# Kernel optimization log

Hardware: AMD Instinct MI355X
Metric: run time of the kernel (lower is better)

## Reference

```python
import jax, jax.numpy as jnp
import numpy as np

B, S, I, H = 64, 512, 512, 1024


def setup_inputs() -> dict:
    key = jax.random.key(0)
    ks = jax.random.split(key, 14)
    bound = (1.0 / H) ** 0.5
    u = lambda k, shape: jax.random.uniform(k, shape, jnp.float32, -bound, bound)
    return {
        "inputs": jax.random.normal(ks[0], (B, S, I), jnp.float32),
        "hidden_states": jax.random.normal(ks[1], (1, B, H), jnp.float32),
        "w_ir": u(ks[2], (H, I)), "w_iz": u(ks[3], (H, I)), "w_in": u(ks[4], (H, I)),
        "b_ir": u(ks[5], (H,)), "b_iz": u(ks[6], (H,)), "b_in": u(ks[7], (H,)),
        "w_hr": u(ks[8], (H, H)), "w_hz": u(ks[9], (H, H)), "w_hn": u(ks[10], (H, H)),
        "b_hr": u(ks[11], (H,)), "b_hz": u(ks[12], (H,)), "b_hn": u(ks[13], (H,)),
    }


def gru_forward(inputs, hidden_states, w_ir, w_iz, w_in, b_ir, b_iz, b_in,
                w_hr, w_hz, w_hn, b_hr, b_hz, b_hn):
    h0 = hidden_states[0]  # (B, H)
    # Original loop starts at t=1, so inputs[:, 0] is unused.
    x = inputs[:, 1:]  # (B, S-1, I)
    # Precompute all input projections (cuDNN-style), then scan the recurrence.
    xr = jnp.einsum('bsi,hi->sbh', x, w_ir) + b_ir
    xz = jnp.einsum('bsi,hi->sbh', x, w_iz) + b_iz
    xn = jnp.einsum('bsi,hi->sbh', x, w_in) + b_in

    def step(h, xs):
        xr_t, xz_t, xn_t = xs
        r = jax.nn.sigmoid(xr_t + h @ w_hr.T + b_hr)
        n = jnp.tanh(xn_t + r * (h @ w_hn.T + b_hn))
        z = jax.nn.sigmoid(xz_t + h @ w_hz.T + b_hz)
        h = (1.0 - z) * n + z * h
        return h, h

    h_last, hs = jax.lax.scan(step, h0, (xr, xz, xn))  # hs: (S-1, B, H)
    outputs = jnp.concatenate([h0[None], hs], axis=0).swapaxes(0, 1)  # (B, S, H)
    return outputs, h_last[None]  # final hidden keeps leading dim 1


def reference(inputs, hidden_states, w_ir, w_iz, w_in, b_ir, b_iz, b_in,
              w_hr, w_hz, w_hn, b_hr, b_hz, b_hn):
    return gru_forward(inputs, hidden_states, w_ir, w_iz, w_in, b_ir, b_iz, b_in,
                       w_hr, w_hz, w_hn, b_hr, b_hz, b_hn)
```

## Files before the change

### kernel.cpp

```cpp
#include <hip/hip_runtime.h>
#include <hip/hip_bf16.h>

typedef __bf16 bf16x8 __attribute__((ext_vector_type(8)));
typedef float  f32x4  __attribute__((ext_vector_type(4)));
typedef unsigned long long ull;

#define Bq 64
#define Sq 512
#define Iq 512
#define Hq 1024
#define TSTEPS 511
#define MB 16
#define NCOLS 32
#define SHq (Sq*Hq)
#define TAGM 0x0001000100010001ull

__device__ inline unsigned short f2bf(float f){ return __builtin_bit_cast(unsigned short, (__bf16)f); }

__device__ inline unsigned ah_addr(unsigned row, unsigned k){ return ((row<<11) + (k<<1)) ^ ((row&7)<<4); }
__device__ inline unsigned ax_addr(unsigned row, unsigned k){ return ((row<<10) + (k<<1)) ^ ((row&7)<<4); }

__device__ inline bf16x8 load_wfrag(const float* p){
  float4 a = *(const float4*)p;
  float4 b = *(const float4*)(p+4);
  bf16x8 w;
  w[0]=(__bf16)a.x; w[1]=(__bf16)a.y; w[2]=(__bf16)a.z; w[3]=(__bf16)a.w;
  w[4]=(__bf16)b.x; w[5]=(__bf16)b.y; w[6]=(__bf16)b.z; w[7]=(__bf16)b.w;
  return w;
}

#define KEEP(v_) asm volatile("" : "+v"(v_))

__global__ __launch_bounds__(512, 1) void gru_kernel(
    const float* __restrict__ x, const float* __restrict__ h0,
    const float* __restrict__ w_ir, const float* __restrict__ w_iz, const float* __restrict__ w_in_,
    const float* __restrict__ b_ir, const float* __restrict__ b_iz, const float* __restrict__ b_in_,
    const float* __restrict__ w_hr, const float* __restrict__ w_hz, const float* __restrict__ w_hn,
    const float* __restrict__ b_hr, const float* __restrict__ b_hz, const float* __restrict__ b_hn,
    float* __restrict__ out, void* ws)
{
  __shared__ unsigned short Ah[MB*Hq];
  __shared__ unsigned short Ax[MB*Iq];
  __shared__ float P[8*2048];
  __shared__ float biasR[NCOLS], biasZ[NCOLS], biasNX[NCOLS], biasNH[NCOLS];

  const unsigned tid    = threadIdx.x;
  const unsigned bid    = blockIdx.x;
  const unsigned g      = bid & 3;
  const unsigned colbase= (bid >> 2) * NCOLS;
  const unsigned lane   = tid & 63;
  const unsigned w      = tid >> 6;
  const unsigned l15    = lane & 15;
  const unsigned l4     = lane >> 4;

  unsigned short* hb0 = (unsigned short*)ws;
  unsigned short* hb1 = hb0 + Bq*Hq;

  if (tid < NCOLS) {
    unsigned c = colbase + tid;
    biasR[tid]  = b_ir[c] + b_hr[c];
    biasZ[tid]  = b_iz[c] + b_hz[c];
    biasNX[tid] = b_in_[c];
    biasNH[tid] = b_hn[c];
  }

  const unsigned ctr = tid >> 8, Lr = (tid >> 2) & 63, ir = tid & 3;
  const unsigned rrow = ((Lr >> 4) << 2) + ir;
  const unsigned rcol = ctr*16 + (Lr & 15);
  float hold;
  {
    unsigned b = g*MB + rrow, hcol = colbase + rcol;
    hold = h0[(size_t)b*Hq + hcol];
    out[(size_t)b*SHq + hcol] = hold;
    unsigned short u = (unsigned short)(f2bf(hold) & ~1u);
    __hip_atomic_store(hb0 + (size_t)b*Hq + hcol, u,
                       __ATOMIC_RELAXED, __HIP_MEMORY_SCOPE_AGENT);
  }

  bf16x8 wRX[2][2], wZX[2][2], wNX[2][2];
  bf16x8 wRH[2][4], wZH[2][4], wNH[2][4];
  #pragma unroll
  for (int ct = 0; ct < 2; ++ct) {
    const unsigned hcf = colbase + ct*16 + l15;
    #pragma unroll
    for (int j = 0; j < 2; ++j) {
      unsigned off = (w*2 + j)*32 + l4*8;
      wRX[ct][j] = load_wfrag(w_ir  + (size_t)hcf*Iq + off);
      wZX[ct][j] = load_wfrag(w_iz  + (size_t)hcf*Iq + off);
      wNX[ct][j] = load_wfrag(w_in_ + (size_t)hcf*Iq + off);
      KEEP(wRX[ct][j]); KEEP(wZX[ct][j]); KEEP(wNX[ct][j]);
    }
    #pragma unroll
    for (int j = 0; j < 4; ++j) {
      unsigned off = (w*4 + j)*32 + l4*8;
      wRH[ct][j] = load_wfrag(w_hr + (size_t)hcf*Hq + off);
      wZH[ct][j] = load_wfrag(w_hz + (size_t)hcf*Hq + off);
      wNH[ct][j] = load_wfrag(w_hn + (size_t)hcf*Hq + off);
      KEEP(wRH[ct][j]); KEEP(wZH[ct][j]); KEEP(wNH[ct][j]);
    }
  }

  const unsigned xcr = lane >> 4, xc16 = lane & 15;
  const unsigned hch = lane & 31, hrb = lane >> 5;

  float4 xpf[4];
  #pragma unroll
  for (int i = 0; i < 4; ++i)
    xpf[i] = *(const float4*)(x + ((size_t)(g*MB + xcr + 4*i)*Sq + 1)*Iq + w*64 + xc16*4);

  for (int t = 0; t < TSTEPS; ++t) {
    const unsigned short* hs = (t & 1) ? hb1 : hb0;
    unsigned short*       hd = (t & 1) ? hb0 : hb1;
    const ull want = ((t >> 1) & 1) ? TAGM : 0ull;
    const unsigned tagd = ((t + 1) >> 1) & 1;

    #pragma unroll
    for (int i = 0; i < 4; ++i) {
      float4 v = xpf[i];
      ull pv = (ull)f2bf(v.x) | ((ull)f2bf(v.y) << 16)
             | ((ull)f2bf(v.z) << 32) | ((ull)f2bf(v.w) << 48);
      *(ull*)((char*)Ax + ax_addr(xcr + 4*i, w*64 + xc16*4)) = pv;
    }

    ull hv[8];
    const unsigned short* hsg = hs + (size_t)(g*MB)*Hq + w*128;
    #pragma unroll
    for (int i = 0; i < 8; ++i)
      hv[i] = __hip_atomic_load((const ull*)(hsg + (size_t)(hrb + 2*i)*Hq) + hch,
                                __ATOMIC_RELAXED, __HIP_MEMORY_SCOPE_AGENT);
    for (;;) {
      unsigned stale = 0;
      #pragma unroll
      for (int i = 0; i < 8; ++i)
        if ((hv[i] & TAGM) != want) stale |= 1u << i;
      if (!stale) break;
      __builtin_amdgcn_s_sleep(1);
      #pragma unroll
      for (int i = 0; i < 8; ++i)
        if (stale & (1u << i))
          hv[i] = __hip_atomic_load((const ull*)(hsg + (size_t)(hrb + 2*i)*Hq) + hch,
                                    __ATOMIC_RELAXED, __HIP_MEMORY_SCOPE_AGENT);
    }

    {
      int tt = (t + 2 <= Sq - 1) ? (t + 2) : (Sq - 1);
      #pragma unroll
      for (int i = 0; i < 4; ++i)
        xpf[i] = *(const float4*)(x + ((size_t)(g*MB + xcr + 4*i)*Sq + (size_t)tt)*Iq + w*64 + xc16*4);
    }

    #pragma unroll
    for (int i = 0; i < 8; ++i)
      *(ull*)((char*)Ah + ah_addr(hrb + 2*i, w*128 + hch*4)) = hv[i];

    f32x4 accR[2]={{0,0,0,0},{0,0,0,0}}, accZ[2]={{0,0,0,0},{0,0,0,0}};
    f32x4 accNX[2]={{0,0,0,0},{0,0,0,0}}, accNH[2]={{0,0,0,0},{0,0,0,0}};
    #pragma unroll
    for (int j = 0; j < 2; ++j) {
      bf16x8 a = *(const bf16x8*)((char*)Ax + ax_addr(l15, (w*2 + j)*32 + l4*8));
      #pragma unroll
      for (int ct = 0; ct < 2; ++ct) {
        accR[ct]  = __builtin_amdgcn_mfma_f32_16x16x32_bf16(a, wRX[ct][j], accR[ct], 0, 0, 0);
        accZ[ct]  = __builtin_amdgcn_mfma_f32_16x16x32_bf16(a, wZX[ct][j], accZ[ct], 0, 0, 0);
        accNX[ct] = __builtin_amdgcn_mfma_f32_16x16x32_bf16(a, wNX[ct][j], accNX[ct], 0, 0, 0);
      }
    }
    #pragma unroll
    for (int j = 0; j < 4; ++j) {
      bf16x8 a = *(const bf16x8*)((char*)Ah + ah_addr(l15, (w*4 + j)*32 + l4*8));
      #pragma unroll
      for (int ct = 0; ct < 2; ++ct) {
        accR[ct]  = __builtin_amdgcn_mfma_f32_16x16x32_bf16(a, wRH[ct][j], accR[ct], 0, 0, 0);
        accZ[ct]  = __builtin_amdgcn_mfma_f32_16x16x32_bf16(a, wZH[ct][j], accZ[ct], 0, 0, 0);
        accNH[ct] = __builtin_amdgcn_mfma_f32_16x16x32_bf16(a, wNH[ct][j], accNH[ct], 0, 0, 0);
      }
    }

    {
      float* pw = P + w*2048 + lane*4;
      #pragma unroll
      for (int ct = 0; ct < 2; ++ct) {
        *(f32x4*)(pw +    0 + ct*256) = accR[ct];
        *(f32x4*)(pw +  512 + ct*256) = accZ[ct];
        *(f32x4*)(pw + 1024 + ct*256) = accNX[ct];
        *(f32x4*)(pw + 1536 + ct*256) = accNH[ct];
      }
    }
    __syncthreads();

    {
      float pr = 0.f, pz = 0.f, pnx = 0.f, pnh = 0.f;
      #pragma unroll
      for (int ww = 0; ww < 8; ++ww) {
        const float* pb = P + ww*2048;
        pr  += pb[tid];
        pz  += pb[512  + tid];
        pnx += pb[1024 + tid];
        pnh += pb[1536 + tid];
      }

      float r = 1.f/(1.f + __expf(-(pr + biasR[rcol])));
      float z = 1.f/(1.f + __expf(-(pz + biasZ[rcol])));
      float nin = pnx + biasNX[rcol] + r*(pnh + biasNH[rcol]);
      float e2 = __expf(2.f*nin);
      float n = 1.f - 2.f/(e2 + 1.f);
      float hn = (1.f - z)*n + z*hold;
      hold = hn;

      const unsigned b = g*MB + rrow, hcol = colbase + rcol;
      unsigned short u = (unsigned short)((f2bf(hn) & ~1u) | tagd);
      __hip_atomic_store(hd + (size_t)b*Hq + hcol, u,
                         __ATOMIC_RELAXED, __HIP_MEMORY_SCOPE_AGENT);
      out[(size_t)b*SHq + (size_t)(t+1)*Hq + hcol] = hn;
      if (t == TSTEPS-1)
        out[(size_t)Bq*SHq + (size_t)b*Hq + hcol] = hn;
    }
    __syncthreads();
  }
}

extern "C" void kernel_launch(void* const* d_in, const int* in_sizes, int n_in,
                              void* d_out, int out_size, void* d_ws, size_t ws_size,
                              hipStream_t stream) {
  const float* x     = (const float*)d_in[0];
  const float* h0    = (const float*)d_in[1];
  const float* w_ir  = (const float*)d_in[2];
  const float* w_iz  = (const float*)d_in[3];
  const float* w_in_ = (const float*)d_in[4];
  const float* b_ir  = (const float*)d_in[5];
  const float* b_iz  = (const float*)d_in[6];
  const float* b_in_ = (const float*)d_in[7];
  const float* w_hr  = (const float*)d_in[8];
  const float* w_hz  = (const float*)d_in[9];
  const float* w_hn  = (const float*)d_in[10];
  const float* b_hr  = (const float*)d_in[11];
  const float* b_hz  = (const float*)d_in[12];
  const float* b_hn  = (const float*)d_in[13];
  float* out = (float*)d_out;

  hipMemsetAsync(d_ws, 0xFF, (size_t)2 * Bq * Hq * sizeof(unsigned short), stream);

  void* args[] = { (void*)&x, (void*)&h0, (void*)&w_ir, (void*)&w_iz, (void*)&w_in_,
                   (void*)&b_ir, (void*)&b_iz, (void*)&b_in_, (void*)&w_hr, (void*)&w_hz,
                   (void*)&w_hn, (void*)&b_hr, (void*)&b_hz, (void*)&b_hn,
                   (void*)&out, (void*)&d_ws };
  hipLaunchCooperativeKernel((void*)gru_kernel, dim3(128), dim3(512), args, 0, stream);
}
```

Measured before the change: 1.295 ms.

## Load hidden state directly into MFMA fragments and poll per k-chunk

Removes the LDS staging buffer for the hidden state. Each lane now atomically loads its MFMA A-fragment straight from global memory, so the LDS write and readback per step are gone. Readiness polling is split per k-chunk and interleaved with the MFMAs, which lets compute on chunks already published start before the rest arrive. In exchange the global loads are now 8-byte pairs in a less coalesced per-row pattern, and a wave-wide __all check replaces the per-lane stale mask.

```diff
diff --git a/kernel.cpp b/kernel.cpp
--- a/kernel.cpp
+++ b/kernel.cpp
@@ -4,6 +4,7 @@
 typedef __bf16 bf16x8 __attribute__((ext_vector_type(8)));
 typedef float  f32x4  __attribute__((ext_vector_type(4)));
 typedef unsigned long long ull;
+typedef ull ull2 __attribute__((ext_vector_type(2)));
 
 #define Bq 64
 #define Sq 512
@@ -17,7 +18,6 @@
 
 __device__ inline unsigned short f2bf(float f){ return __builtin_bit_cast(unsigned short, (__bf16)f); }
 
-__device__ inline unsigned ah_addr(unsigned row, unsigned k){ return ((row<<11) + (k<<1)) ^ ((row&7)<<4); }
 __device__ inline unsigned ax_addr(unsigned row, unsigned k){ return ((row<<10) + (k<<1)) ^ ((row&7)<<4); }
 
 __device__ inline bf16x8 load_wfrag(const float* p){
@@ -39,7 +39,6 @@
     const float* __restrict__ b_hr, const float* __restrict__ b_hz, const float* __restrict__ b_hn,
     float* __restrict__ out, void* ws)
 {
-  __shared__ unsigned short Ah[MB*Hq];
   __shared__ unsigned short Ax[MB*Iq];
   __shared__ float P[8*2048];
   __shared__ float biasR[NCOLS], biasZ[NCOLS], biasNX[NCOLS], biasNH[NCOLS];
@@ -101,7 +100,6 @@
   }
 
   const unsigned xcr = lane >> 4, xc16 = lane & 15;
-  const unsigned hch = lane & 31, hrb = lane >> 5;
 
   float4 xpf[4];
   #pragma unroll
@@ -122,24 +120,12 @@
       *(ull*)((char*)Ax + ax_addr(xcr + 4*i, w*64 + xc16*4)) = pv;
     }
 
-    ull hv[8];
-    const unsigned short* hsg = hs + (size_t)(g*MB)*Hq + w*128;
-    #pragma unroll
-    for (int i = 0; i < 8; ++i)
-      hv[i] = __hip_atomic_load((const ull*)(hsg + (size_t)(hrb + 2*i)*Hq) + hch,
-                                __ATOMIC_RELAXED, __HIP_MEMORY_SCOPE_AGENT);
-    for (;;) {
-      unsigned stale = 0;
-      #pragma unroll
-      for (int i = 0; i < 8; ++i)
-        if ((hv[i] & TAGM) != want) stale |= 1u << i;
-      if (!stale) break;
-      __builtin_amdgcn_s_sleep(1);
-      #pragma unroll
-      for (int i = 0; i < 8; ++i)
-        if (stale & (1u << i))
-          hv[i] = __hip_atomic_load((const ull*)(hsg + (size_t)(hrb + 2*i)*Hq) + hch,
-                                    __ATOMIC_RELAXED, __HIP_MEMORY_SCOPE_AGENT);
+    ull hv[4][2];
+    const ull* hrow = (const ull*)(hs + (size_t)(g*MB + l15)*Hq + w*128 + l4*8);
+    #pragma unroll
+    for (int j = 0; j < 4; ++j) {
+      hv[j][0] = __hip_atomic_load(hrow + j*8,     __ATOMIC_RELAXED, __HIP_MEMORY_SCOPE_AGENT);
+      hv[j][1] = __hip_atomic_load(hrow + j*8 + 1, __ATOMIC_RELAXED, __HIP_MEMORY_SCOPE_AGENT);
     }
 
     {
@@ -148,10 +134,6 @@
       for (int i = 0; i < 4; ++i)
         xpf[i] = *(const float4*)(x + ((size_t)(g*MB + xcr + 4*i)*Sq + (size_t)tt)*Iq + w*64 + xc16*4);
     }
-
-    #pragma unroll
-    for (int i = 0; i < 8; ++i)
-      *(ull*)((char*)Ah + ah_addr(hrb + 2*i, w*128 + hch*4)) = hv[i];
 
     f32x4 accR[2]={{0,0,0,0},{0,0,0,0}}, accZ[2]={{0,0,0,0},{0,0,0,0}};
     f32x4 accNX[2]={{0,0,0,0},{0,0,0,0}}, accNH[2]={{0,0,0,0},{0,0,0,0}};
@@ -165,9 +147,20 @@
         accNX[ct] = __builtin_amdgcn_mfma_f32_16x16x32_bf16(a, wNX[ct][j], accNX[ct], 0, 0, 0);
       }
     }
+
     #pragma unroll
     for (int j = 0; j < 4; ++j) {
-      bf16x8 a = *(const bf16x8*)((char*)Ah + ah_addr(l15, (w*4 + j)*32 + l4*8));
+      for (;;) {
+        int ok = ((hv[j][0] & TAGM) == want) && ((hv[j][1] & TAGM) == want);
+        if (__all(ok)) break;
+        __builtin_amdgcn_s_sleep(1);
+        if ((hv[j][0] & TAGM) != want)
+          hv[j][0] = __hip_atomic_load(hrow + j*8,     __ATOMIC_RELAXED, __HIP_MEMORY_SCOPE_AGENT);
+        if ((hv[j][1] & TAGM) != want)
+          hv[j][1] = __hip_atomic_load(hrow + j*8 + 1, __ATOMIC_RELAXED, __HIP_MEMORY_SCOPE_AGENT);
+      }
+      ull2 hp; hp[0] = hv[j][0]; hp[1] = hv[j][1];
+      bf16x8 a = __builtin_bit_cast(bf16x8, hp);
       #pragma unroll
       for (int ct = 0; ct < 2; ++ct) {
         accR[ct]  = __builtin_amdgcn_mfma_f32_16x16x32_bf16(a, wRH[ct][j], accR[ct], 0, 0, 0);
```

Result: slower. 1.892 ms (+46.1%).
